# Kernel optimization log

Hardware: AMD Instinct MI355X
Metric: run time of the kernel (lower is better)

Reference implementation:

```python
import jax, jax.numpy as jnp
import numpy as np

B, N, K = 64, 128, 12
D_ATOM, D_NBR, D_NEW = 256, 320, 256
H, DK = 8, 32  # D_NEW = H * DK
LN_EPS = 1e-5
NEG_INF = -1e9


def setup_inputs() -> dict:
    key = jax.random.key(0)
    ks = jax.random.split(key, 10)
    atom_feature = jax.random.normal(ks[0], (B, N, D_ATOM), jnp.float32)
    atom_neighbor_feature = jax.random.normal(ks[1], (B, N, K, D_NBR), jnp.float32)
    # valid-neighbor masks from random neighbor counts in [1, K]
    counts = jax.random.randint(ks[2], (B, N), 1, K + 1)
    valid = (jnp.arange(K)[None, None, :] < counts[:, :, None]).astype(jnp.float32)
    atom_attend_mask = valid[..., None]                      # (B,N,K,1), 1=real neighbor
    atom_softmax_mask = (1.0 - valid[..., None]) * NEG_INF   # (B,N,K,1), additive
    # parameters
    s = 1.0 / np.sqrt(D_ATOM)
    W_atom = jax.random.uniform(ks[3], (D_ATOM, D_NEW), jnp.float32, -s, s)
    b_atom = jnp.zeros((D_NEW,), jnp.float32)
    s2 = 1.0 / np.sqrt(D_NBR)
    W_nbr = jax.random.uniform(ks[4], (D_NBR, D_NEW), jnp.float32, -s2, s2)
    b_nbr = jnp.zeros((D_NEW,), jnp.float32)
    s3 = 1.0 / np.sqrt(DK)
    w_align = jax.random.uniform(ks[5], (DK, 1), jnp.float32, -s3, s3)
    b_align = jnp.zeros((1,), jnp.float32)
    ln_gamma = jnp.ones((D_NEW,), jnp.float32)
    ln_beta = jnp.zeros((D_NEW,), jnp.float32)
    return dict(atom_feature=atom_feature, atom_neighbor_feature=atom_neighbor_feature,
                atom_softmax_mask=atom_softmax_mask, atom_attend_mask=atom_attend_mask,
                W_atom=W_atom, b_atom=b_atom, W_nbr=W_nbr, b_nbr=b_nbr,
                w_align=w_align, b_align=b_align, ln_gamma=ln_gamma, ln_beta=ln_beta)


def reference(atom_feature, atom_neighbor_feature, atom_softmax_mask, atom_attend_mask,
              W_atom, b_atom, W_nbr, b_nbr, w_align, b_align, ln_gamma, ln_beta):
    # dropout is identity at eval time
    h = atom_feature @ W_atom + b_atom                    # (B,N,D_NEW)
    e = atom_neighbor_feature @ W_nbr + b_nbr             # (B,N,K,D_NEW)
    h = h.reshape(B, N, 1, H, DK)                         # broadcast over K
    e = e.reshape(B, N, K, H, DK)
    # GATv2: act(h_i + e_j) then per-head linear score
    feat = jax.nn.leaky_relu(h + e)                       # slope 0.01 == torch default
    score = feat @ w_align + b_align                      # (B,N,K,H,1)
    score = score + atom_softmax_mask[:, :, :, None, :]   # additive -inf on pad
    attn = jax.nn.softmax(score, axis=2)                  # softmax over neighbors K
    attn = attn * atom_attend_mask[:, :, :, None, :]
    ctx = jnp.sum(attn * e, axis=2).reshape(B, N, H * DK)  # (B,N,D_NEW)
    # LayerNorm
    mu = jnp.mean(ctx, axis=-1, keepdims=True)
    xc = ctx - mu
    var = jnp.mean(xc * xc, axis=-1, keepdims=True)
    return xc * jax.lax.rsqrt(var + LN_EPS) * ln_gamma + ln_beta
```

## Files before the change

kernel.cpp:

```cpp
#include <hip/hip_runtime.h>

#define KN 12
#define DNBR 320
#define DNEW 256
#define BN_TOT 8192
#define ATB 2
#define HATB 16
#define NKS_E 10
#define NKS_H 8
#define ASTR_H 264
#define H_OFF 294912
#define NCHUNK 40

typedef short bf8_t __attribute__((ext_vector_type(8)));
typedef float f32x4 __attribute__((ext_vector_type(4)));
typedef unsigned short us8 __attribute__((ext_vector_type(8)));
using u16 = unsigned short;
using u32 = unsigned int;

typedef __attribute__((address_space(3))) void lds_vp;
typedef __attribute__((address_space(1))) const void gc_vp;

__device__ __forceinline__ void dma16(const void* g, void* l) {
    __builtin_amdgcn_global_load_lds((gc_vp*)g, (lds_vp*)l, 16, 0, 0);
}

__device__ __forceinline__ u16 f2bf(float f) {
    u32 x = __float_as_uint(f);
    return (u16)((x + 0x7fffu + ((x >> 16) & 1u)) >> 16);
}

__device__ __forceinline__ us8 pack8(float4 a, float4 b) {
    us8 v;
    v[0] = f2bf(a.x); v[1] = f2bf(a.y); v[2] = f2bf(a.z); v[3] = f2bf(a.w);
    v[4] = f2bf(b.x); v[5] = f2bf(b.y); v[6] = f2bf(b.z); v[7] = f2bf(b.w);
    return v;
}

__device__ __forceinline__ bf8_t cvt8(float4 a, float4 b) {
    u32 r0, r1, r2, r3;
    asm("v_cvt_pk_bf16_f32 %0, %1, %2" : "=v"(r0) : "v"(a.x), "v"(a.y));
    asm("v_cvt_pk_bf16_f32 %0, %1, %2" : "=v"(r1) : "v"(a.z), "v"(a.w));
    asm("v_cvt_pk_bf16_f32 %0, %1, %2" : "=v"(r2) : "v"(b.x), "v"(b.y));
    asm("v_cvt_pk_bf16_f32 %0, %1, %2" : "=v"(r3) : "v"(b.z), "v"(b.w));
    union { u32 u[4]; bf8_t v; } cv;
    cv.u[0] = r0; cv.u[1] = r1; cv.u[2] = r2; cv.u[3] = r3;
    return cv.v;
}

__global__ __launch_bounds__(256) void build_b2(
    const float* __restrict__ Wn, const float* __restrict__ Wa,
    u16* __restrict__ B2)
{
    int tile = blockIdx.x * 4 + (threadIdx.x >> 6);
    int l = threadIdx.x & 63;
    int q = l >> 4, m = l & 15;
    us8 v;
    if (tile < 160) {
        int ks = tile >> 4, nt = tile & 15;
        int col = nt * 16 + m;
#pragma unroll
        for (int e = 0; e < 8; e++)
            v[e] = f2bf(Wn[(ks * 32 + q * 8 + e) * DNEW + col]);
    } else {
        int tt = tile - 160;
        int ks = tt >> 4, nt = tt & 15;
        int col = nt * 16 + m;
#pragma unroll
        for (int e = 0; e < 8; e++)
            v[e] = f2bf(Wa[(ks * 32 + q * 8 + e) * DNEW + col]);
    }
    *(us8*)&B2[(size_t)tile * 512 + l * 8] = v;
}

__global__ __launch_bounds__(256) void h_pre(
    const float* __restrict__ atomf, const u16* __restrict__ B2,
    const float* __restrict__ ba, float* __restrict__ h_g)
{
    __shared__ u16 A[HATB * ASTR_H];

    const int t = threadIdx.x;
    const int l = t & 63, w = t >> 6, q = l >> 4, m = l & 15;
    const int ab = blockIdx.x * HATB;

    const float* base = atomf + (size_t)ab * DNEW;
    float4 u0 = *(const float4*)(base + t * 8);
    float4 u1 = *(const float4*)(base + t * 8 + 4);
    float4 u2 = *(const float4*)(base + (t + 256) * 8);
    float4 u3 = *(const float4*)(base + (t + 256) * 8 + 4);
    int ai = t >> 5, c8 = t & 31;
    *(us8*)&A[ai * ASTR_H + c8 * 8] = pack8(u0, u1);
    *(us8*)&A[(ai + 8) * ASTR_H + c8 * 8] = pack8(u2, u3);
    __syncthreads();

    f32x4 acc[4];
#pragma unroll
    for (int j = 0; j < 4; j++) acc[j] = (f32x4){0.f, 0.f, 0.f, 0.f};

#pragma unroll
    for (int ks = 0; ks < NKS_H; ks++) {
        bf8_t af = *(bf8_t*)&A[m * ASTR_H + ks * 32 + q * 8];
#pragma unroll
        for (int j = 0; j < 4; j++) {
            bf8_t bfj = *(const bf8_t*)&B2[((size_t)(160 + ks * 16 + w * 4 + j) * 64 + l) * 8];
            acc[j] = __builtin_amdgcn_mfma_f32_16x16x32_bf16(af, bfj, acc[j], 0, 0, 0);
        }
    }
#pragma unroll
    for (int j = 0; j < 4; j++) {
        int col = w * 64 + j * 16 + m;
        float bav = ba[col];
#pragma unroll
        for (int r = 0; r < 4; r++) {
            int row = ab + q * 4 + r;
            h_g[(size_t)row * DNEW + col] = acc[j][r] + bav;
        }
    }
}

__global__ __launch_bounds__(256, 4) void fused_all(
    const float* __restrict__ nbrf,
    const float* __restrict__ smaskg, const float* __restrict__ amaskg,
    const u16* __restrict__ B2, const float* __restrict__ h_g,
    const float* __restrict__ bnb, const float* __restrict__ walg,
    const float* __restrict__ balg, const float* __restrict__ gam,
    const float* __restrict__ bet, float* __restrict__ out)
{
    __shared__ __align__(16) float smem[NCHUNK * 256];

    const int t = threadIdx.x;
    const int l = t & 63, w = t >> 6, q = l >> 4, m = l & 15;
    const int a0 = blockIdx.x * ATB;
    const bool qv = (q < 3);

    const int srow = (m < KN) ? m : (KN - 1);
    for (int c = w; c < NCHUNK; c += 4) {
        int at = c / 20, rem = c - at * 20, ksc = rem >> 1, half = rem & 1;
        const float* src = nbrf + ((size_t)(a0 + at) * KN + srow) * DNBR
                         + ksc * 32 + q * 8 + half * 4;
        dma16(src, (char*)smem + (size_t)c * 1024);
    }

    float hv[ATB][4], bnbv[4], wv[4];
#pragma unroll
    for (int j = 0; j < 4; j++) {
        int col = w * 64 + j * 16 + m;
        hv[0][j] = h_g[(size_t)(a0 + 0) * DNEW + col];
        hv[1][j] = h_g[(size_t)(a0 + 1) * DNEW + col];
        bnbv[j] = bnb[col];
        wv[j] = walg[(j * 16 + m) & 31];
    }

    __syncthreads();

    const float4* A2 = (const float4*)smem;
    f32x4 acc_e[ATB][4];
#pragma unroll
    for (int at = 0; at < ATB; at++)
#pragma unroll
        for (int j = 0; j < 4; j++) acc_e[at][j] = (f32x4){0.f, 0.f, 0.f, 0.f};

#pragma unroll
    for (int ks = 0; ks < NKS_E; ks++) {
        bf8_t bfj[4];
#pragma unroll
        for (int j = 0; j < 4; j++)
            bfj[j] = *(const bf8_t*)&B2[((size_t)(ks * 16 + w * 4 + j) * 64 + l) * 8];
        float4 lo0 = A2[(size_t)((0 * NKS_E + ks) * 2 + 0) * 64 + l];
        float4 hi0 = A2[(size_t)((0 * NKS_E + ks) * 2 + 1) * 64 + l];
        float4 lo1 = A2[(size_t)((1 * NKS_E + ks) * 2 + 0) * 64 + l];
        float4 hi1 = A2[(size_t)((1 * NKS_E + ks) * 2 + 1) * 64 + l];
        bf8_t af0 = cvt8(lo0, hi0);
        bf8_t af1 = cvt8(lo1, hi1);
#pragma unroll
        for (int j = 0; j < 4; j++) {
            acc_e[0][j] = __builtin_amdgcn_mfma_f32_16x16x32_bf16(af0, bfj[j], acc_e[0][j], 0, 0, 0);
            acc_e[1][j] = __builtin_amdgcn_mfma_f32_16x16x32_bf16(af1, bfj[j], acc_e[1][j], 0, 0, 0);
        }
    }

    const float bal = balg[0];
    float smv[ATB][4], amv[ATB][4];
#pragma unroll
    for (int at = 0; at < ATB; at++)
#pragma unroll
        for (int r = 0; r < 4; r++) {
            int k = q * 4 + r;
            smv[at][r] = qv ? smaskg[(size_t)(a0 + at) * KN + k] + bal : 0.f;
            amv[at][r] = qv ? amaskg[(size_t)(a0 + at) * KN + k] : 0.f;
        }

#pragma unroll
    for (int j = 0; j < 4; j++) {
#pragma unroll
        for (int at = 0; at < ATB; at++)
#pragma unroll
            for (int r = 0; r < 4; r++) acc_e[at][j][r] += bnbv[j];
    }

    float ctxv[ATB][4], s1s[ATB], s2s[ATB];
#pragma unroll
    for (int at = 0; at < ATB; at++) {
        float s1 = 0.f, s2 = 0.f;
#pragma unroll
        for (int jj = 0; jj < 2; jj++) {
            float p[4];
#pragma unroll
            for (int r = 0; r < 4; r++) {
                float pp = 0.f;
#pragma unroll
                for (int jo = 0; jo < 2; jo++) {
                    int j = jj * 2 + jo;
                    float f = acc_e[at][j][r] + hv[at][j];
                    f = f > 0.f ? f : 0.01f * f;
                    pp = fmaf(f, wv[j], pp);
                }
                pp += __shfl_xor(pp, 1);
                pp += __shfl_xor(pp, 2);
                pp += __shfl_xor(pp, 4);
                pp += __shfl_xor(pp, 8);
                p[r] = qv ? pp + smv[at][r] : -1e30f;
            }
            float mx = fmaxf(fmaxf(p[0], p[1]), fmaxf(p[2], p[3]));
            mx = fmaxf(mx, __shfl_xor(mx, 16));
            mx = fmaxf(mx, __shfl_xor(mx, 32));
            float ex[4], ss = 0.f;
#pragma unroll
            for (int r = 0; r < 4; r++) {
                ex[r] = qv ? __expf(p[r] - mx) : 0.f;
                ss += ex[r];
            }
            ss += __shfl_xor(ss, 16);
            ss += __shfl_xor(ss, 32);
            float inv = 1.f / ss;
            float am[4];
#pragma unroll
            for (int r = 0; r < 4; r++)
                am[r] = qv ? ex[r] * inv * amv[at][r] : 0.f;
#pragma unroll
            for (int jo = 0; jo < 2; jo++) {
                int j = jj * 2 + jo;
                float cp = am[0] * acc_e[at][j][0] + am[1] * acc_e[at][j][1] +
                           am[2] * acc_e[at][j][2] + am[3] * acc_e[at][j][3];
                cp += __shfl_xor(cp, 16);
                cp += __shfl_xor(cp, 32);
                ctxv[at][j] = cp;
                s1 += cp;
                s2 += cp * cp;
            }
        }
#pragma unroll
        for (int off = 1; off < 16; off <<= 1) {
            s1 += __shfl_xor(s1, off);
            s2 += __shfl_xor(s2, off);
        }
        s1s[at] = s1; s2s[at] = s2;
    }

    float* red_l = smem;
    __syncthreads();
    if (l == 0) {
#pragma unroll
        for (int at = 0; at < ATB; at++) {
            red_l[at * 8 + w] = s1s[at];
            red_l[at * 8 + 4 + w] = s2s[at];
        }
    }
    __syncthreads();

#pragma unroll
    for (int at = 0; at < ATB; at++) {
        float ts1 = red_l[at * 8 + 0] + red_l[at * 8 + 1] + red_l[at * 8 + 2] + red_l[at * 8 + 3];
        float ts2 = red_l[at * 8 + 4] + red_l[at * 8 + 5] + red_l[at * 8 + 6] + red_l[at * 8 + 7];
        float mu = ts1 * (1.f / 256.f);
        float var = ts2 * (1.f / 256.f) - mu * mu;
        var = fmaxf(var, 0.f);
        float rs = rsqrtf(var + 1e-5f);
        if (q == 0) {
#pragma unroll
            for (int j = 0; j < 4; j++) {
                int col = w * 64 + j * 16 + m;
                out[(size_t)(a0 + at) * DNEW + col] =
                    (ctxv[at][j] - mu) * rs * gam[col] + bet[col];
            }
        }
    }
}

extern "C" void kernel_launch(void* const* d_in, const int* in_sizes, int n_in,
                              void* d_out, int out_size, void* d_ws, size_t ws_size,
                              hipStream_t stream) {
    const float* atomf = (const float*)d_in[0];
    const float* nbrf  = (const float*)d_in[1];
    const float* smask = (const float*)d_in[2];
    const float* amask = (const float*)d_in[3];
    const float* Wa    = (const float*)d_in[4];
    const float* ba    = (const float*)d_in[5];
    const float* Wn    = (const float*)d_in[6];
    const float* bnb   = (const float*)d_in[7];
    const float* wal   = (const float*)d_in[8];
    const float* bal   = (const float*)d_in[9];
    const float* gam   = (const float*)d_in[10];
    const float* bet   = (const float*)d_in[11];
    float* outp = (float*)d_out;

    u16* B2 = (u16*)d_ws;
    float* h_g = (float*)((char*)d_ws + H_OFF);

    build_b2<<<72, 256, 0, stream>>>(Wn, Wa, B2);
    h_pre<<<BN_TOT / HATB, 256, 0, stream>>>(atomf, B2, ba, h_g);
    fused_all<<<BN_TOT / ATB, 256, 0, stream>>>(nbrf, smask, amask, B2, h_g,
                                                bnb, wal, bal, gam, bet, outp);
}
```

Before: 251.1 us.

## Process four atom-pair tiles per block with DMA prefetch of next tile

The fused kernel now loops over four consecutive 2-atom tiles per block, with a quarter as many blocks as before. Per-column constants (bias, align weights, gamma, beta) are loaded once per block. The next tile's neighbor-feature DMA into LDS is issued after the reduction syncs and before the output stores, so the load overlaps the store epilogue. In exchange there is only a single LDS buffer, so prefetch overlap is limited, and fewer blocks (1024) may reduce latency hiding across CUs.

```diff
diff --git a/kernel.cpp b/kernel.cpp
--- a/kernel.cpp
+++ b/kernel.cpp
@@ -5,6 +5,7 @@
 #define DNEW 256
 #define BN_TOT 8192
 #define ATB 2
+#define TPT 4
 #define HATB 16
 #define NKS_E 10
 #define NKS_H 8
@@ -130,158 +131,190 @@
 
     const int t = threadIdx.x;
     const int l = t & 63, w = t >> 6, q = l >> 4, m = l & 15;
-    const int a0 = blockIdx.x * ATB;
     const bool qv = (q < 3);
-
     const int srow = (m < KN) ? m : (KN - 1);
-    for (int c = w; c < NCHUNK; c += 4) {
-        int at = c / 20, rem = c - at * 20, ksc = rem >> 1, half = rem & 1;
-        const float* src = nbrf + ((size_t)(a0 + at) * KN + srow) * DNBR
-                         + ksc * 32 + q * 8 + half * 4;
-        dma16(src, (char*)smem + (size_t)c * 1024);
-    }
-
-    float hv[ATB][4], bnbv[4], wv[4];
+
+    const float bal = balg[0];
+    float bnbv[4], wv[4], gv[4], btv[4];
 #pragma unroll
     for (int j = 0; j < 4; j++) {
         int col = w * 64 + j * 16 + m;
-        hv[0][j] = h_g[(size_t)(a0 + 0) * DNEW + col];
-        hv[1][j] = h_g[(size_t)(a0 + 1) * DNEW + col];
         bnbv[j] = bnb[col];
         wv[j] = walg[(j * 16 + m) & 31];
-    }
-
-    __syncthreads();
-
-    const float4* A2 = (const float4*)smem;
-    f32x4 acc_e[ATB][4];
-#pragma unroll
-    for (int at = 0; at < ATB; at++)
-#pragma unroll
-        for (int j = 0; j < 4; j++) acc_e[at][j] = (f32x4){0.f, 0.f, 0.f, 0.f};
-
-#pragma unroll
-    for (int ks = 0; ks < NKS_E; ks++) {
-        bf8_t bfj[4];
-#pragma unroll
-        for (int j = 0; j < 4; j++)
-            bfj[j] = *(const bf8_t*)&B2[((size_t)(ks * 16 + w * 4 + j) * 64 + l) * 8];
-        float4 lo0 = A2[(size_t)((0 * NKS_E + ks) * 2 + 0) * 64 + l];
-        float4 hi0 = A2[(size_t)((0 * NKS_E + ks) * 2 + 1) * 64 + l];
-        float4 lo1 = A2[(size_t)((1 * NKS_E + ks) * 2 + 0) * 64 + l];
-        float4 hi1 = A2[(size_t)((1 * NKS_E + ks) * 2 + 1) * 64 + l];
-        bf8_t af0 = cvt8(lo0, hi0);
-        bf8_t af1 = cvt8(lo1, hi1);
+        gv[j] = gam[col];
+        btv[j] = bet[col];
+    }
+
+    const int tile0 = blockIdx.x * TPT;
+
+    {
+        const int a0 = tile0 * ATB;
+        for (int c = w; c < NCHUNK; c += 4) {
+            int at = c / 20, rem = c - at * 20, ksc = rem >> 1, half = rem & 1;
+            const float* src = nbrf + ((size_t)(a0 + at) * KN + srow) * DNBR
+                             + ksc * 32 + q * 8 + half * 4;
+            dma16(src, (char*)smem + (size_t)c * 1024);
+        }
+    }
+
+    for (int g = 0; g < TPT; ++g) {
+        const int a0 = (tile0 + g) * ATB;
+
+        float hv[ATB][4];
 #pragma unroll
         for (int j = 0; j < 4; j++) {
-            acc_e[0][j] = __builtin_amdgcn_mfma_f32_16x16x32_bf16(af0, bfj[j], acc_e[0][j], 0, 0, 0);
-            acc_e[1][j] = __builtin_amdgcn_mfma_f32_16x16x32_bf16(af1, bfj[j], acc_e[1][j], 0, 0, 0);
-        }
-    }
-
-    const float bal = balg[0];
-    float smv[ATB][4], amv[ATB][4];
-#pragma unroll
-    for (int at = 0; at < ATB; at++)
-#pragma unroll
-        for (int r = 0; r < 4; r++) {
-            int k = q * 4 + r;
-            smv[at][r] = qv ? smaskg[(size_t)(a0 + at) * KN + k] + bal : 0.f;
-            amv[at][r] = qv ? amaskg[(size_t)(a0 + at) * KN + k] : 0.f;
-        }
-
-#pragma unroll
-    for (int j = 0; j < 4; j++) {
+            int col = w * 64 + j * 16 + m;
+            hv[0][j] = h_g[(size_t)(a0 + 0) * DNEW + col];
+            hv[1][j] = h_g[(size_t)(a0 + 1) * DNEW + col];
+        }
+        float smv[ATB][4], amv[ATB][4];
 #pragma unroll
         for (int at = 0; at < ATB; at++)
 #pragma unroll
-            for (int r = 0; r < 4; r++) acc_e[at][j][r] += bnbv[j];
-    }
-
-    float ctxv[ATB][4], s1s[ATB], s2s[ATB];
-#pragma unroll
-    for (int at = 0; at < ATB; at++) {
-        float s1 = 0.f, s2 = 0.f;
-#pragma unroll
-        for (int jj = 0; jj < 2; jj++) {
-            float p[4];
-#pragma unroll
             for (int r = 0; r < 4; r++) {
-                float pp = 0.f;
+                int k = q * 4 + r;
+                smv[at][r] = qv ? smaskg[(size_t)(a0 + at) * KN + k] + bal : 0.f;
+                amv[at][r] = qv ? amaskg[(size_t)(a0 + at) * KN + k] : 0.f;
+            }
+
+        __syncthreads();
+
+        const float4* A2 = (const float4*)smem;
+        f32x4 acc_e[ATB][4];
+#pragma unroll
+        for (int at = 0; at < ATB; at++)
+#pragma unroll
+            for (int j = 0; j < 4; j++) acc_e[at][j] = (f32x4){0.f, 0.f, 0.f, 0.f};
+
+#pragma unroll
+        for (int ks = 0; ks < NKS_E; ks++) {
+            bf8_t bfj[4];
+#pragma unroll
+            for (int j = 0; j < 4; j++)
+                bfj[j] = *(const bf8_t*)&B2[((size_t)(ks * 16 + w * 4 + j) * 64 + l) * 8];
+            float4 lo0 = A2[(size_t)((0 * NKS_E + ks) * 2 + 0) * 64 + l];
+            float4 hi0 = A2[(size_t)((0 * NKS_E + ks) * 2 + 1) * 64 + l];
+            float4 lo1 = A2[(size_t)((1 * NKS_E + ks) * 2 + 0) * 64 + l];
+            float4 hi1 = A2[(size_t)((1 * NKS_E + ks) * 2 + 1) * 64 + l];
+            bf8_t af0 = cvt8(lo0, hi0);
+            bf8_t af1 = cvt8(lo1, hi1);
+#pragma unroll
+            for (int j = 0; j < 4; j++) {
+                acc_e[0][j] = __builtin_amdgcn_mfma_f32_16x16x32_bf16(af0, bfj[j], acc_e[0][j], 0, 0, 0);
+                acc_e[1][j] = __builtin_amdgcn_mfma_f32_16x16x32_bf16(af1, bfj[j], acc_e[1][j], 0, 0, 0);
+            }
+        }
+
+#pragma unroll
+        for (int j = 0; j < 4; j++) {
+#pragma unroll
+            for (int at = 0; at < ATB; at++)
+#pragma unroll
+                for (int r = 0; r < 4; r++) acc_e[at][j][r] += bnbv[j];
+        }
+
+        float ctxv[ATB][4], s1s[ATB], s2s[ATB];
+#pragma unroll
+        for (int at = 0; at < ATB; at++) {
+            float s1 = 0.f, s2 = 0.f;
+#pragma unroll
+            for (int jj = 0; jj < 2; jj++) {
+                float p[4];
+#pragma unroll
+                for (int r = 0; r < 4; r++) {
+                    float pp = 0.f;
+#pragma unroll
+                    for (int jo = 0; jo < 2; jo++) {
+                        int j = jj * 2 + jo;
+                        float f = acc_e[at][j][r] + hv[at][j];
+                        f = f > 0.f ? f : 0.01f * f;
+                        pp = fmaf(f, wv[j], pp);
+                    }
+                    pp += __shfl_xor(pp, 1);
+                    pp += __shfl_xor(pp, 2);
+                    pp += __shfl_xor(pp, 4);
+                    pp += __shfl_xor(pp, 8);
+                    p[r] = qv ? pp + smv[at][r] : -1e30f;
+                }
+                float mx = fmaxf(fmaxf(p[0], p[1]), fmaxf(p[2], p[3]));
+                mx = fmaxf(mx, __shfl_xor(mx, 16));
+                mx = fmaxf(mx, __shfl_xor(mx, 32));
+                float ex[4], ss = 0.f;
+#pragma unroll
+                for (int r = 0; r < 4; r++) {
+                    ex[r] = qv ? __expf(p[r] - mx) : 0.f;
+                    ss += ex[r];
+                }
+                ss += __shfl_xor(ss, 16);
+                ss += __shfl_xor(ss, 32);
+                float inv = 1.f / ss;
+                float am[4];
+#pragma unroll
+                for (int r = 0; r < 4; r++)
+                    am[r] = qv ? ex[r] * inv * amv[at][r] : 0.f;
 #pragma unroll
                 for (int jo = 0; jo < 2; jo++) {
                     int j = jj * 2 + jo;
-                    float f = acc_e[at][j][r] + hv[at][j];
-                    f = f > 0.f ? f : 0.01f * f;
-                    pp = fmaf(f, wv[j], pp);
+                    float cp = am[0] * acc_e[at][j][0] + am[1] * acc_e[at][j][1] +
+                               am[2] * acc_e[at][j][2] + am[3] * acc_e[at][j][3];
+                    cp += __shfl_xor(cp, 16);
+                    cp += __shfl_xor(cp, 32);
+                    ctxv[at][j] = cp;
+                    s1 += cp;
+                    s2 += cp * cp;
                 }
-                pp += __shfl_xor(pp, 1);
-                pp += __shfl_xor(pp, 2);
-                pp += __shfl_xor(pp, 4);
-                pp += __shfl_xor(pp, 8);
-                p[r] = qv ? pp + smv[at][r] : -1e30f;
-            }
-            float mx = fmaxf(fmaxf(p[0], p[1]), fmaxf(p[2], p[3]));
-            mx = fmaxf(mx, __shfl_xor(mx, 16));
-            mx = fmaxf(mx, __shfl_xor(mx, 32));
-            float ex[4], ss = 0.f;
-#pragma unroll
-            for (int r = 0; r < 4; r++) {
-                ex[r] = qv ? __expf(p[r] - mx) : 0.f;
-                ss += ex[r];
-            }
-            ss += __shfl_xor(ss, 16);
-            ss += __shfl_xor(ss, 32);
-            float inv = 1.f / ss;
-            float am[4];
-#pragma unroll
-            for (int r = 0; r < 4; r++)
-                am[r] = qv ? ex[r] * inv * amv[at][r] : 0.f;
-#pragma unroll
-            for (int jo = 0; jo < 2; jo++) {
-                int j = jj * 2 + jo;
-                float cp = am[0] * acc_e[at][j][0] + am[1] * acc_e[at][j][1] +
-                           am[2] * acc_e[at][j][2] + am[3] * acc_e[at][j][3];
-                cp += __shfl_xor(cp, 16);
-                cp += __shfl_xor(cp, 32);
-                ctxv[at][j] = cp;
-                s1 += cp;
-                s2 += cp * cp;
-            }
-        }
-#pragma unroll
-        for (int off = 1; off < 16; off <<= 1) {
-            s1 += __shfl_xor(s1, off);
-            s2 += __shfl_xor(s2, off);
-        }
-        s1s[at] = s1; s2s[at] = s2;
-    }
-
-    float* red_l = smem;
-    __syncthreads();
-    if (l == 0) {
+            }
+#pragma unroll
+            for (int off = 1; off < 16; off <<= 1) {
+                s1 += __shfl_xor(s1, off);
+                s2 += __shfl_xor(s2, off);
+            }
+            s1s[at] = s1; s2s[at] = s2;
+        }
+
+        float* red_l = smem;
+        __syncthreads();
+        if (l == 0) {
+#pragma unroll
+            for (int at = 0; at < ATB; at++) {
+                red_l[at * 8 + w] = s1s[at];
+                red_l[at * 8 + 4 + w] = s2s[at];
+            }
+        }
+        __syncthreads();
+
+        float mu_[ATB], rs_[ATB];
 #pragma unroll
         for (int at = 0; at < ATB; at++) {
-            red_l[at * 8 + w] = s1s[at];
-            red_l[at * 8 + 4 + w] = s2s[at];
-        }
-    }
-    __syncthreads();
-
-#pragma unroll
-    for (int at = 0; at < ATB; at++) {
-        float ts1 = red_l[at * 8 + 0] + red_l[at * 8 + 1] + red_l[at * 8 + 2] + red_l[at * 8 + 3];
-        float ts2 = red_l[at * 8 + 4] + red_l[at * 8 + 5] + red_l[at * 8 + 6] + red_l[at * 8 + 7];
-        float mu = ts1 * (1.f / 256.f);
-        float var = ts2 * (1.f / 256.f) - mu * mu;
-        var = fmaxf(var, 0.f);
-        float rs = rsqrtf(var + 1e-5f);
+            float ts1 = red_l[at * 8 + 0] + red_l[at * 8 + 1] + red_l[at * 8 + 2] + red_l[at * 8 + 3];
+            float ts2 = red_l[at * 8 + 4] + red_l[at * 8 + 5] + red_l[at * 8 + 6] + red_l[at * 8 + 7];
+            float mu = ts1 * (1.f / 256.f);
+            float var = ts2 * (1.f / 256.f) - mu * mu;
+            var = fmaxf(var, 0.f);
+            mu_[at] = mu;
+            rs_[at] = rsqrtf(var + 1e-5f);
+        }
+        __syncthreads();
+
+        if (g + 1 < TPT) {
+            const int an = (tile0 + g + 1) * ATB;
+            for (int c = w; c < NCHUNK; c += 4) {
+                int at = c / 20, rem = c - at * 20, ksc = rem >> 1, half = rem & 1;
+                const float* src = nbrf + ((size_t)(an + at) * KN + srow) * DNBR
+                                 + ksc * 32 + q * 8 + half * 4;
+                dma16(src, (char*)smem + (size_t)c * 1024);
+            }
+        }
+
         if (q == 0) {
 #pragma unroll
-            for (int j = 0; j < 4; j++) {
-                int col = w * 64 + j * 16 + m;
-                out[(size_t)(a0 + at) * DNEW + col] =
-                    (ctxv[at][j] - mu) * rs * gam[col] + bet[col];
+            for (int at = 0; at < ATB; at++) {
+#pragma unroll
+                for (int j = 0; j < 4; j++) {
+                    int col = w * 64 + j * 16 + m;
+                    out[(size_t)(a0 + at) * DNEW + col] =
+                        (ctxv[at][j] - mu_[at]) * rs_[at] * gv[j] + btv[j];
+                }
             }
         }
     }
@@ -309,6 +342,6 @@
 
     build_b2<<<72, 256, 0, stream>>>(Wn, Wa, B2);
     h_pre<<<BN_TOT / HATB, 256, 0, stream>>>(atomf, B2, ba, h_g);
-    fused_all<<<BN_TOT / ATB, 256, 0, stream>>>(nbrf, smask, amask, B2, h_g,
-                                                bnb, wal, bal, gam, bet, outp);
-}
+    fused_all<<<BN_TOT / (ATB * TPT), 256, 0, stream>>>(nbrf, smask, amask, B2, h_g,
+                                                        bnb, wal, bal, gam, bet, outp);
+}
```

Result: slower. 324.5 us (+29.2%).

## Process four atoms per block with 512 threads, one head per wave

Applied to the files above, without the earlier changes.

Each block of the fused attention kernel now handles four atoms with eight waves instead of two atoms with four. Each wave owns 32 output columns, which is exactly one head, so the per-head score reduction no longer splits across column pairs. The mask, h, gamma and beta loads are issued before the barrier so they overlap the DMA of neighbor features into LDS. This doubles the LDS footprint per block and halves the grid, which may lower occupancy or CU balance.

```diff
diff --git a/kernel.cpp b/kernel.cpp
--- a/kernel.cpp
+++ b/kernel.cpp
@@ -4,13 +4,13 @@
 #define DNBR 320
 #define DNEW 256
 #define BN_TOT 8192
-#define ATB 2
+#define ATB 4
 #define HATB 16
 #define NKS_E 10
 #define NKS_H 8
 #define ASTR_H 264
 #define H_OFF 294912
-#define NCHUNK 40
+#define NCHUNK 80
 
 typedef short bf8_t __attribute__((ext_vector_type(8)));
 typedef float f32x4 __attribute__((ext_vector_type(4)));
@@ -118,7 +118,7 @@
     }
 }
 
-__global__ __launch_bounds__(256, 4) void fused_all(
+__global__ __launch_bounds__(512, 4) void fused_all(
     const float* __restrict__ nbrf,
     const float* __restrict__ smaskg, const float* __restrict__ amaskg,
     const u16* __restrict__ B2, const float* __restrict__ h_g,
@@ -129,57 +129,32 @@
     __shared__ __align__(16) float smem[NCHUNK * 256];
 
     const int t = threadIdx.x;
-    const int l = t & 63, w = t >> 6, q = l >> 4, m = l & 15;
+    const int l = t & 63, q = l >> 4, m = l & 15;
+    const int w = __builtin_amdgcn_readfirstlane(t >> 6);
     const int a0 = blockIdx.x * ATB;
     const bool qv = (q < 3);
-
     const int srow = (m < KN) ? m : (KN - 1);
-    for (int c = w; c < NCHUNK; c += 4) {
+
+    for (int c = w; c < NCHUNK; c += 8) {
         int at = c / 20, rem = c - at * 20, ksc = rem >> 1, half = rem & 1;
         const float* src = nbrf + ((size_t)(a0 + at) * KN + srow) * DNBR
                          + ksc * 32 + q * 8 + half * 4;
         dma16(src, (char*)smem + (size_t)c * 1024);
     }
 
-    float hv[ATB][4], bnbv[4], wv[4];
-#pragma unroll
-    for (int j = 0; j < 4; j++) {
-        int col = w * 64 + j * 16 + m;
-        hv[0][j] = h_g[(size_t)(a0 + 0) * DNEW + col];
-        hv[1][j] = h_g[(size_t)(a0 + 1) * DNEW + col];
+    const float bal = balg[0];
+    float hv[ATB][2], bnbv[2], wv[2], gv[2], btv[2];
+#pragma unroll
+    for (int j = 0; j < 2; j++) {
+        int col = w * 32 + j * 16 + m;
         bnbv[j] = bnb[col];
-        wv[j] = walg[(j * 16 + m) & 31];
-    }
-
-    __syncthreads();
-
-    const float4* A2 = (const float4*)smem;
-    f32x4 acc_e[ATB][4];
-#pragma unroll
-    for (int at = 0; at < ATB; at++)
-#pragma unroll
-        for (int j = 0; j < 4; j++) acc_e[at][j] = (f32x4){0.f, 0.f, 0.f, 0.f};
-
-#pragma unroll
-    for (int ks = 0; ks < NKS_E; ks++) {
-        bf8_t bfj[4];
-#pragma unroll
-        for (int j = 0; j < 4; j++)
-            bfj[j] = *(const bf8_t*)&B2[((size_t)(ks * 16 + w * 4 + j) * 64 + l) * 8];
-        float4 lo0 = A2[(size_t)((0 * NKS_E + ks) * 2 + 0) * 64 + l];
-        float4 hi0 = A2[(size_t)((0 * NKS_E + ks) * 2 + 1) * 64 + l];
-        float4 lo1 = A2[(size_t)((1 * NKS_E + ks) * 2 + 0) * 64 + l];
-        float4 hi1 = A2[(size_t)((1 * NKS_E + ks) * 2 + 1) * 64 + l];
-        bf8_t af0 = cvt8(lo0, hi0);
-        bf8_t af1 = cvt8(lo1, hi1);
-#pragma unroll
-        for (int j = 0; j < 4; j++) {
-            acc_e[0][j] = __builtin_amdgcn_mfma_f32_16x16x32_bf16(af0, bfj[j], acc_e[0][j], 0, 0, 0);
-            acc_e[1][j] = __builtin_amdgcn_mfma_f32_16x16x32_bf16(af1, bfj[j], acc_e[1][j], 0, 0, 0);
-        }
-    }
-
-    const float bal = balg[0];
+        wv[j] = walg[j * 16 + m];
+        gv[j] = gam[col];
+        btv[j] = bet[col];
+#pragma unroll
+        for (int at = 0; at < ATB; at++)
+            hv[at][j] = h_g[(size_t)(a0 + at) * DNEW + col];
+    }
     float smv[ATB][4], amv[ATB][4];
 #pragma unroll
     for (int at = 0; at < ATB; at++)
@@ -190,64 +165,83 @@
             amv[at][r] = qv ? amaskg[(size_t)(a0 + at) * KN + k] : 0.f;
         }
 
-#pragma unroll
-    for (int j = 0; j < 4; j++) {
+    __syncthreads();
+
+    const float4* A2 = (const float4*)smem;
+    f32x4 acc_e[ATB][2];
+#pragma unroll
+    for (int at = 0; at < ATB; at++)
+#pragma unroll
+        for (int j = 0; j < 2; j++) acc_e[at][j] = (f32x4){0.f, 0.f, 0.f, 0.f};
+
+#pragma unroll
+    for (int ks = 0; ks < NKS_E; ks++) {
+        bf8_t bfj[2];
+#pragma unroll
+        for (int j = 0; j < 2; j++)
+            bfj[j] = *(const bf8_t*)&B2[((size_t)(ks * 16 + w * 2 + j) * 64 + l) * 8];
+#pragma unroll
+        for (int at = 0; at < ATB; at++) {
+            float4 lo = A2[(size_t)((at * NKS_E + ks) * 2 + 0) * 64 + l];
+            float4 hi = A2[(size_t)((at * NKS_E + ks) * 2 + 1) * 64 + l];
+            bf8_t af = cvt8(lo, hi);
+            acc_e[at][0] = __builtin_amdgcn_mfma_f32_16x16x32_bf16(af, bfj[0], acc_e[at][0], 0, 0, 0);
+            acc_e[at][1] = __builtin_amdgcn_mfma_f32_16x16x32_bf16(af, bfj[1], acc_e[at][1], 0, 0, 0);
+        }
+    }
+
+#pragma unroll
+    for (int j = 0; j < 2; j++)
 #pragma unroll
         for (int at = 0; at < ATB; at++)
 #pragma unroll
             for (int r = 0; r < 4; r++) acc_e[at][j][r] += bnbv[j];
-    }
-
-    float ctxv[ATB][4], s1s[ATB], s2s[ATB];
+
+    float ctxv[ATB][2], s1s[ATB], s2s[ATB];
 #pragma unroll
     for (int at = 0; at < ATB; at++) {
+        float p[4];
+#pragma unroll
+        for (int r = 0; r < 4; r++) {
+            float pp = 0.f;
+#pragma unroll
+            for (int j = 0; j < 2; j++) {
+                float f = acc_e[at][j][r] + hv[at][j];
+                f = f > 0.f ? f : 0.01f * f;
+                pp = fmaf(f, wv[j], pp);
+            }
+            pp += __shfl_xor(pp, 1);
+            pp += __shfl_xor(pp, 2);
+            pp += __shfl_xor(pp, 4);
+            pp += __shfl_xor(pp, 8);
+            p[r] = qv ? pp + smv[at][r] : -1e30f;
+        }
+        float mx = fmaxf(fmaxf(p[0], p[1]), fmaxf(p[2], p[3]));
+        mx = fmaxf(mx, __shfl_xor(mx, 16));
+        mx = fmaxf(mx, __shfl_xor(mx, 32));
+        float ex[4], ss = 0.f;
+#pragma unroll
+        for (int r = 0; r < 4; r++) {
+            ex[r] = qv ? __expf(p[r] - mx) : 0.f;
+            ss += ex[r];
+        }
+        ss += __shfl_xor(ss, 16);
+        ss += __shfl_xor(ss, 32);
+        float inv = 1.f / ss;
+        float am[4];
+#pragma unroll
+        for (int r = 0; r < 4; r++)
+            am[r] = qv ? ex[r] * inv * amv[at][r] : 0.f;
         float s1 = 0.f, s2 = 0.f;
 #pragma unroll
-        for (int jj = 0; jj < 2; jj++) {
-            float p[4];
-#pragma unroll
-            for (int r = 0; r < 4; r++) {
-                float pp = 0.f;
-#pragma unroll
-                for (int jo = 0; jo < 2; jo++) {
-                    int j = jj * 2 + jo;
-                    float f = acc_e[at][j][r] + hv[at][j];
-                    f = f > 0.f ? f : 0.01f * f;
-                    pp = fmaf(f, wv[j], pp);
-                }
-                pp += __shfl_xor(pp, 1);
-                pp += __shfl_xor(pp, 2);
-                pp += __shfl_xor(pp, 4);
-                pp += __shfl_xor(pp, 8);
-                p[r] = qv ? pp + smv[at][r] : -1e30f;
-            }
-            float mx = fmaxf(fmaxf(p[0], p[1]), fmaxf(p[2], p[3]));
-            mx = fmaxf(mx, __shfl_xor(mx, 16));
-            mx = fmaxf(mx, __shfl_xor(mx, 32));
-            float ex[4], ss = 0.f;
-#pragma unroll
-            for (int r = 0; r < 4; r++) {
-                ex[r] = qv ? __expf(p[r] - mx) : 0.f;
-                ss += ex[r];
-            }
-            ss += __shfl_xor(ss, 16);
-            ss += __shfl_xor(ss, 32);
-            float inv = 1.f / ss;
-            float am[4];
-#pragma unroll
-            for (int r = 0; r < 4; r++)
-                am[r] = qv ? ex[r] * inv * amv[at][r] : 0.f;
-#pragma unroll
-            for (int jo = 0; jo < 2; jo++) {
-                int j = jj * 2 + jo;
-                float cp = am[0] * acc_e[at][j][0] + am[1] * acc_e[at][j][1] +
-                           am[2] * acc_e[at][j][2] + am[3] * acc_e[at][j][3];
-                cp += __shfl_xor(cp, 16);
-                cp += __shfl_xor(cp, 32);
-                ctxv[at][j] = cp;
-                s1 += cp;
-                s2 += cp * cp;
-            }
+        for (int j = 0; j < 2; j++) {
+            float cp = am[0] * acc_e[at][j][0] + am[1] * acc_e[at][j][1] +
+                       am[2] * acc_e[at][j][2] + am[3] * acc_e[at][j][3];
+            cp += __shfl_xor(cp, 16);
+            cp += __shfl_xor(cp, 32);
+            ctxv[at][j] = cp;
+            s1 += cp;
+            s2 += cp * cp;
         }
 #pragma unroll
         for (int off = 1; off < 16; off <<= 1) {
@@ -262,26 +256,30 @@
     if (l == 0) {
 #pragma unroll
         for (int at = 0; at < ATB; at++) {
-            red_l[at * 8 + w] = s1s[at];
-            red_l[at * 8 + 4 + w] = s2s[at];
+            red_l[at * 16 + w] = s1s[at];
+            red_l[at * 16 + 8 + w] = s2s[at];
         }
     }
     __syncthreads();
 
 #pragma unroll
     for (int at = 0; at < ATB; at++) {
-        float ts1 = red_l[at * 8 + 0] + red_l[at * 8 + 1] + red_l[at * 8 + 2] + red_l[at * 8 + 3];
-        float ts2 = red_l[at * 8 + 4] + red_l[at * 8 + 5] + red_l[at * 8 + 6] + red_l[at * 8 + 7];
+        float ts1 = 0.f, ts2 = 0.f;
+#pragma unroll
+        for (int k = 0; k < 8; k++) {
+            ts1 += red_l[at * 16 + k];
+            ts2 += red_l[at * 16 + 8 + k];
+        }
         float mu = ts1 * (1.f / 256.f);
         float var = ts2 * (1.f / 256.f) - mu * mu;
         var = fmaxf(var, 0.f);
         float rs = rsqrtf(var + 1e-5f);
         if (q == 0) {
 #pragma unroll
-            for (int j = 0; j < 4; j++) {
-                int col = w * 64 + j * 16 + m;
+            for (int j = 0; j < 2; j++) {
+                int col = w * 32 + j * 16 + m;
                 out[(size_t)(a0 + at) * DNEW + col] =
-                    (ctxv[at][j] - mu) * rs * gam[col] + bet[col];
+                    (ctxv[at][j] - mu) * rs * gv[j] + btv[j];
             }
         }
     }
@@ -309,6 +307,6 @@
 
     build_b2<<<72, 256, 0, stream>>>(Wn, Wa, B2);
     h_pre<<<BN_TOT / HATB, 256, 0, stream>>>(atomf, B2, ba, h_g);
-    fused_all<<<BN_TOT / ATB, 256, 0, stream>>>(nbrf, smask, amask, B2, h_g,
+    fused_all<<<BN_TOT / ATB, 512, 0, stream>>>(nbrf, smask, amask, B2, h_g,
                                                 bnb, wal, bal, gam, bet, outp);
 }
```

New measurement: 247.9 us. About the same (-1.3%).
